# Kernel optimization log

Hardware: AMD Instinct MI355X
Metric: run time of the kernel (lower is better)

Reference implementation:

```python
import math
import jax, jax.numpy as jnp
from jax import lax
import numpy as np

jax.config.update("jax_enable_x64", True)  # original uses complex128 FFTs

MS_H = 5
MS_W = 5
EPS = 1e-8


def setup_inputs() -> dict:
    H = W = 512
    B = 32
    rng = np.random.default_rng(0)
    i = np.arange(H, dtype=np.float64)[:, None]
    j = np.arange(W, dtype=np.float64)[None, :]
    # smooth, strictly-positive template so NCC peak neighborhood is log-safe
    template = (2.0
                + np.exp(-(((i - H / 2) ** 2 + (j - W / 2) ** 2) / (2 * (H / 8.0) ** 2)))
                + 0.5 * np.cos(2 * np.pi * 3 * i / H) * np.cos(2 * np.pi * 5 * j / W)
                + 0.3 * np.sin(2 * np.pi * 7 * j / W + 1.0) * np.cos(2 * np.pi * 2 * i / H)
                ).astype(np.float32)
    frames = np.empty((B, H, W), np.float32)
    for b in range(B):
        dx, dy = rng.integers(-3, 4, size=2)
        frames[b] = np.roll(template, (int(dx), int(dy)), axis=(0, 1))
    frames += 0.02 * rng.standard_normal((B, H, W)).astype(np.float32)
    fr = jnp.asarray(frames)[None, :, :, :, None]  # [1, B, H, W, 1]
    return {"fr": fr, "template": jnp.asarray(template)}


def reference(fr, template):
    B = fr.shape[1]
    H, W = template.shape
    # ---- normalize_template ----
    template_zm = template - jnp.mean(template)
    template_var = jnp.sum(jnp.square(template_zm)) + EPS  # scalar
    # fft3d of [H,W,1] == 2D FFT over (H,W)
    target_freq = jnp.fft.fft2(template_zm.astype(jnp.complex128))  # [H,W]

    imgs = fr[0]  # [B,H,W,1]
    # ---- normalize_image ----
    k0, k1 = H - 2 * MS_W, W - 2 * MS_H
    imgs_zm = imgs - jnp.mean(imgs, axis=(1, 2), keepdims=True)
    x = imgs[:, :, :, 0]
    img_stack = jnp.stack([x, jnp.square(x)], axis=3)  # [B,H,W,2]
    localsum = lax.reduce_window(img_stack, jnp.array(0.0, img_stack.dtype), lax.add,
                                 (1, k0, k1, 1), (1, 1, 1, 1), 'VALID') / (k0 * k1)
    ls = localsum[:, :, :, 0:1]      # avg(x)   [B,11,11,1]
    ls_sq = localsum[:, :, :, 1:2]   # avg(x^2)
    imgs_var = ls_sq - jnp.square(ls) / (k0 * k1) + EPS
    imgs_var = jnp.where(imgs_var < 0, 0.0, imgs_var)

    denominator = jnp.sqrt(template_var * imgs_var)  # [B,11,11,1]

    # ---- FFT cross-correlation (fft3d over (batch,H,W) as in TF) ----
    fr_freq = jnp.fft.fftn(imgs_zm[:, :, :, 0].astype(jnp.complex128), axes=(0, 1, 2))
    img_product = fr_freq * jnp.conj(target_freq)[None]
    cc = jnp.abs(jnp.fft.ifftn(img_product, axes=(0, 1, 2))).astype(jnp.float32)
    rolled = jnp.roll(cc, (B, H // 2, W // 2), axis=(0, 1, 2))
    nominator = rolled[:, H // 2 - MS_W:H // 2 + MS_W + 1,
                       W // 2 - MS_H:W // 2 + MS_H + 1, None]  # [B,11,11,1]

    ncc = nominator / denominator
    ncc = jnp.where(jnp.isnan(ncc), 0.0, ncc)

    # ---- extract_fractional_peak ----
    Y = 2 * MS_H + 1
    nc = ncc[..., 0]  # [B,11,11]
    am = jnp.argmax(nc.reshape(B, -1), axis=1)
    sh_xi = am // Y
    sh_yi = am % Y
    sh_x_n = -(sh_xi - MS_H).astype(jnp.float32)
    sh_y_n = -(sh_yi - MS_W).astype(jnp.float32)
    l = jnp.log(nc)
    bb = jnp.arange(B)
    log_xm1_y = l[bb, sh_xi - 1, sh_yi]
    log_xp1_y = l[bb, sh_xi + 1, sh_yi]
    log_x_ym1 = l[bb, sh_xi, sh_yi - 1]
    log_x_yp1 = l[bb, sh_xi, sh_yi + 1]
    four_log_xy = 4.0 * l[bb, sh_xi, sh_yi]
    sh_x_n = sh_x_n - (log_xm1_y - log_xp1_y) / (2 * log_xm1_y - four_log_xy + 2 * log_xp1_y)
    sh_y_n = sh_y_n - (log_x_ym1 - log_x_yp1) / (2 * log_x_ym1 - four_log_xy + 2 * log_x_yp1)
    sh_x = sh_x_n  # [B]
    sh_y = sh_y_n

    # ---- apply_shifts_dft_tf(fr[0], [-sh_x, -sh_y]) ----
    # shifts tuple becomes (-sh_y, -sh_x, 0); sh_0 uses -shifts[0]=sh_y with Nr, sh_1 uses sh_x with Nc
    Nr = jnp.fft.ifftshift(jnp.arange(-math.floor(W / 2.0), math.ceil(W / 2.0))).astype(jnp.float32)  # [W]
    Nc = jnp.fft.ifftshift(jnp.arange(-math.floor(H / 2.0), math.ceil(H / 2.0))).astype(jnp.float32)  # [H]
    sh_tot = (sh_y[:, None, None] * Nr[None, None, :] / W
              + sh_x[:, None, None] * Nc[None, :, None] / H)  # [B,H,W]
    src_freq = jnp.fft.fftn(fr[0, :, :, :, 0].astype(jnp.complex128), axes=(1, 2))
    Greg = src_freq * jnp.exp(-1j * 2.0 * math.pi * sh_tot.astype(jnp.complex128))
    new_img = jnp.real(jnp.fft.ifftn(Greg, axes=(1, 2))).astype(jnp.float32)  # [B,H,W]

    out = jnp.transpose(new_img, (0, 2, 1)).reshape(B, H * W)
    return out
```

## Files before the change

### kernel.cpp

```cpp
#include <hip/hip_runtime.h>
#include <hip/hip_bf16.h>
#include <math.h>

#define NPIX 262144
#define PI_D 3.14159265358979323846264338327950288

typedef __attribute__((ext_vector_type(8))) short v8s;
typedef __attribute__((ext_vector_type(4))) float v4f;
typedef __attribute__((ext_vector_type(4))) unsigned short v4u;


__device__ inline unsigned short f2bf(float x){ return __bfloat16_as_ushort(__float2bfloat16(x)); }
__device__ inline float bf2f(unsigned short h){ return __bfloat162float(__ushort_as_bfloat16(h)); }

__global__ __launch_bounds__(256) void k_stats_part(const float* __restrict__ t, double* __restrict__ part){
    int base = blockIdx.x * 4096;
    double s = 0.0, s2 = 0.0;
    #pragma unroll
    for (int k = 0; k < 4; ++k){
        float4 v = *(const float4*)&t[base + k*1024 + threadIdx.x*4];
        s  += (double)v.x + (double)v.y + (double)v.z + (double)v.w;
        s2 += (double)v.x*v.x + (double)v.y*v.y + (double)v.z*v.z + (double)v.w*v.w;
    }
    __shared__ double rs[256], rs2[256];
    rs[threadIdx.x] = s; rs2[threadIdx.x] = s2; __syncthreads();
    for (int off = 128; off > 0; off >>= 1){
        if (threadIdx.x < off){ rs[threadIdx.x] += rs[threadIdx.x+off]; rs2[threadIdx.x] += rs2[threadIdx.x+off]; }
        __syncthreads();
    }
    if (threadIdx.x == 0){ part[blockIdx.x*2] = rs[0]; part[blockIdx.x*2+1] = rs2[0]; }
}

__global__ __launch_bounds__(64) void k_stats_final(const double* __restrict__ part, double* __restrict__ stats){
    double s = part[threadIdx.x*2], s2 = part[threadIdx.x*2+1];
    #pragma unroll
    for (int off = 32; off > 0; off >>= 1){
        s  += __shfl_down(s, off);
        s2 += __shfl_down(s2, off);
    }
    if (threadIdx.x == 0){
        stats[0] = s / (double)NPIX;
        stats[1] = s2 - s*s/(double)NPIX + 1e-8;
    }
}

__global__ __launch_bounds__(256) void k_tsplit(const float* __restrict__ tpl, const double* __restrict__ stats,
                                                unsigned short* __restrict__ tsp){
    float mean = (float)stats[0];
    int base = blockIdx.x * 1024 + threadIdx.x * 4;
    float4 v = *(const float4*)&tpl[base];
    v.x -= mean; v.y -= mean; v.z -= mean; v.w -= mean;
    unsigned short h0 = f2bf(v.x), h1 = f2bf(v.y), h2 = f2bf(v.z), h3 = f2bf(v.w);
    v4u hv = {h0, h1, h2, h3};
    v4u lv = {f2bf(v.x - bf2f(h0)), f2bf(v.y - bf2f(h1)), f2bf(v.z - bf2f(h2)), f2bf(v.w - bf2f(h3))};
    *(v4u*)&tsp[base] = hv;
    *(v4u*)&tsp[262144 + base] = lv;
}

__global__ __launch_bounds__(256) void k_winfin(const float* __restrict__ fr, const float* __restrict__ csum,
                                                const float* __restrict__ csum2, const double* __restrict__ stats,
                                                double* __restrict__ den){
    int b = blockIdx.x;
    const float* img = fr + (size_t)b * NPIX;
    __shared__ double fc[512], fc2[512];
    __shared__ double rsum[20], rsum2[20];
    __shared__ float E[20][20], E2[20][20];
    __shared__ double red[256], red2[256];
    int t = threadIdx.x;
    for (int c = t; c < 512; c += 256){
        double s = 0.0, s2 = 0.0;
        for (int k = 0; k < 64; ++k){
            size_t o = ((size_t)(b*64 + k) << 9) + c;
            s += (double)csum[o]; s2 += (double)csum2[o];
        }
        fc[c] = s; fc2[c] = s2;
    }
    if (t < 400){
        int i = t / 20, j = t % 20;
        int row = (i < 10) ? i : (i + 492);
        int col = (j < 10) ? j : (j + 492);
        float v = img[(row<<9) + col];
        E[i][j] = v; E2[i][j] = v*v;
    }
    __syncthreads();
    red[t] = fc[t] + fc[t+256];
    red2[t] = fc2[t] + fc2[t+256];
    __syncthreads();
    for (int off = 128; off > 0; off >>= 1){
        if (t < off){ red[t] += red[t+off]; red2[t] += red2[t+off]; }
        __syncthreads();
    }
    double F1 = red[0], F2 = red2[0];
    int lane = t & 63, wv = t >> 6;
    for (int e = wv; e < 20; e += 4){
        int row = (e < 10) ? e : (e + 492);
        double s = 0.0, s2 = 0.0;
        for (int c = lane; c < 512; c += 64){
            float v = img[(row<<9) + c];
            s += v; s2 += (double)v*v;
        }
        #pragma unroll
        for (int off = 32; off > 0; off >>= 1){ s += __shfl_down(s, off); s2 += __shfl_down(s2, off); }
        if (lane == 0){ rsum[e] = s; rsum2[e] = s2; }
    }
    __syncthreads();
    if (t < 121){
        int u = t / 11, v = t % 11;
        double S1 = F1, S2 = F2;
        for (int i = 0; i < u; ++i){ S1 -= rsum[i]; S2 -= rsum2[i]; }
        for (int k = 10+u; k < 20; ++k){ S1 -= rsum[k]; S2 -= rsum2[k]; }
        for (int j = 0; j < v; ++j){
            double cw = fc[j], cq = fc2[j];
            for (int i = 0; i < u; ++i){ cw -= E[i][j]; cq -= E2[i][j]; }
            for (int k = 10+u; k < 20; ++k){ cw -= E[k][j]; cq -= E2[k][j]; }
            S1 -= cw; S2 -= cq;
        }
        for (int jj = 10+v; jj < 20; ++jj){
            int col = jj + 492;
            double cw = fc[col], cq = fc2[col];
            for (int i = 0; i < u; ++i){ cw -= E[i][jj]; cq -= E2[i][jj]; }
            for (int k = 10+u; k < 20; ++k){ cw -= E[k][jj]; cq -= E2[k][jj]; }
            S1 -= cw; S2 -= cq;
        }
        const double K = 502.0*502.0;
        double ivar = S2/K - (S1*S1)/(K*K*K) + 1e-8;
        if (ivar < 0.0) ivar = 0.0;
        den[b*121 + u*11 + v] = sqrt(stats[1] * ivar);
    }
}

__global__ __launch_bounds__(256, 2) void k_ncc(const float* __restrict__ fr,
                                                const unsigned short* __restrict__ tsp,
                                                float* __restrict__ partial,
                                                float* __restrict__ csum, float* __restrict__ csum2,
                                                double* __restrict__ snn_part){
    int b = blockIdx.x >> 6, chunk = blockIdx.x & 63;
    int i0 = chunk << 3;
    int tid = threadIdx.x;
    __shared__ unsigned short Th[24][520], Tl[24][520];
    __shared__ unsigned short Xh[8][544], Xl[8][544];
    __shared__ float Dred[4][16][16];
    __shared__ double snred[4];
    for (int q = tid; q < 1536; q += 256){
        int r = q >> 6, c8 = (q & 63) << 3;
        int grow = (i0 - 5 + r + 512) & 511;
        *(float4*)&Th[r][c8] = *(const float4*)&tsp[((size_t)grow << 9) + c8];
        *(float4*)&Tl[r][c8] = *(const float4*)&tsp[262144 + ((size_t)grow << 9) + c8];
    }
    const float* img = fr + ((size_t)b << 18);
    for (int q = tid; q < 1088; q += 256){
        int r = q / 136, qq = q - r*136;
        int col = ((qq << 2) - 16) & 511;
        float4 v = *(const float4*)&img[((size_t)(i0 + r) << 9) + col];
        unsigned short h0 = f2bf(v.x), h1 = f2bf(v.y), h2 = f2bf(v.z), h3 = f2bf(v.w);
        v4u hv = {h0, h1, h2, h3};
        v4u lv = {f2bf(v.x - bf2f(h0)), f2bf(v.y - bf2f(h1)), f2bf(v.z - bf2f(h2)), f2bf(v.w - bf2f(h3))};
        *(v4u*)&Xh[r][qq << 2] = hv;
        *(v4u*)&Xl[r][qq << 2] = lv;
    }
    __syncthreads();
    int l = tid & 63, wv = tid >> 6;
    {
        int c0 = tid << 1;
        float s0=0.f, q0=0.f, s1=0.f, q1=0.f;
        double sn = 0.0;
        #pragma unroll
        for (int r = 0; r < 8; ++r){
            unsigned uh = *(const unsigned*)&Xh[r][c0 + 16];
            unsigned ul = *(const unsigned*)&Xl[r][c0 + 16];
            float v0 = bf2f((unsigned short)uh) + bf2f((unsigned short)ul);
            float v1 = bf2f((unsigned short)(uh >> 16)) + bf2f((unsigned short)(ul >> 16));
            s0 += v0; q0 += v0*v0; s1 += v1; q1 += v1*v1;
            float d = v0 - v1;
            sn += ((i0 + r) & 1) ? -(double)d : (double)d;
        }
        size_t o = ((size_t)(b*64 + chunk) << 9) + c0;
        float2 cs = {s0, s1}, cq = {q0, q1};
        *(float2*)&csum[o] = cs;
        *(float2*)&csum2[o] = cq;
        #pragma unroll
        for (int off = 32; off > 0; off >>= 1) sn += __shfl_down(sn, off);
        if (l == 0) snred[wv] = sn;
    }
    int lr = l & 15, lk = l >> 4;
    v4f acc = (v4f){0.f, 0.f, 0.f, 0.f};
    union UB { unsigned u[4]; v8s s; };
    int sbase = (lk << 3) - lr + 21;
    unsigned sh = (unsigned)((sbase & 1) << 4);
    #pragma unroll
    for (int ii = 0; ii < 2; ++ii){
        int ro = 2*wv + ii;
        const unsigned* xh32 = (const unsigned*)&Xh[ro][0];
        const unsigned* xl32 = (const unsigned*)&Xl[ro][0];
        #pragma unroll 1
        for (int ks = 0; ks < 16; ++ks){
            int ka = (ks << 5) + (lk << 3);
            v8s ah = *(v8s*)&Th[ro + lr][ka];
            v8s al = *(v8s*)&Tl[ro + lr][ka];
            int W = ((ks << 5) + sbase) >> 1;
            unsigned wh[5], wl[5];
            #pragma unroll
            for (int j = 0; j < 5; ++j){ wh[j] = xh32[W + j]; wl[j] = xl32[W + j]; }
            UB bh, bl;
            #pragma unroll
            for (int j = 0; j < 4; ++j){
                bh.u[j] = __builtin_amdgcn_alignbit(wh[j+1], wh[j], sh);
                bl.u[j] = __builtin_amdgcn_alignbit(wl[j+1], wl[j], sh);
            }
            acc = __builtin_amdgcn_mfma_f32_16x16x32_bf16(ah, bh.s, acc, 0, 0, 0);
            acc = __builtin_amdgcn_mfma_f32_16x16x32_bf16(al, bh.s, acc, 0, 0, 0);
            acc = __builtin_amdgcn_mfma_f32_16x16x32_bf16(ah, bl.s, acc, 0, 0, 0);
        }
    }
    #pragma unroll
    for (int r = 0; r < 4; ++r) Dred[wv][4*lk + r][lr] = acc[r];
    __syncthreads();
    if (tid < 121){
        int s0 = tid / 11, s1 = tid - s0*11;
        int dy = 10 - s0, dx = 10 - s1;
        partial[(size_t)(b*64 + chunk)*121 + tid] =
            Dred[0][dy][dx] + Dred[1][dy][dx] + Dred[2][dy][dx] + Dred[3][dy][dx];
    }
    if (tid == 0)
        snn_part[b*64 + chunk] = snred[0] + snred[1] + snred[2] + snred[3];
}

__global__ __launch_bounds__(128) void k_shifts(const float* __restrict__ partial, const double* __restrict__ den,
                                                const double* __restrict__ snn_part, double* __restrict__ shx,
                                                double* __restrict__ shy, float* __restrict__ c2){
    int b = blockIdx.x;
    __shared__ double l[121], nc[121];
    for (int e = threadIdx.x; e < 121; e += 128){
        double s = 0.0;
        for (int c = 0; c < 64; ++c) s += (double)partial[(size_t)(b*64 + c)*121 + e];
        double nom = fabs(s);
        double v = nom / den[b*121 + e];
        if (v != v) v = 0.0;
        nc[e] = v;
        l[e] = log(v);
    }
    __syncthreads();
    if (threadIdx.x == 0){
        int am = 0; double best = nc[0];
        for (int e = 1; e < 121; ++e) if (nc[e] > best){ best = nc[e]; am = e; }
        int u = am / 11, v = am % 11;
        double sx = -(double)(u - 5), sy = -(double)(v - 5);
        int um1 = u - 1; if (um1 < 0) um1 += 11; if (um1 > 10) um1 = 10;
        int up1 = u + 1; if (up1 > 10) up1 = 10;
        int vm1 = v - 1; if (vm1 < 0) vm1 += 11; if (vm1 > 10) vm1 = 10;
        int vp1 = v + 1; if (vp1 > 10) vp1 = 10;
        double l0x4 = 4.0 * l[u*11 + v];
        double lm = l[um1*11 + v], lp = l[up1*11 + v];
        sx -= (lm - lp) / (2.0*lm - l0x4 + 2.0*lp);
        double lm2 = l[u*11 + vm1], lp2 = l[u*11 + vp1];
        sy -= (lm2 - lp2) / (2.0*lm2 - l0x4 + 2.0*lp2);
        shx[b] = sx; shy[b] = sy;
        double snn = 0.0;
        for (int c = 0; c < 64; ++c) snn += snn_part[b*64 + c];
        double kx = sin(PI_D * sx) / 512.0, ky = sin(PI_D * sy) / 512.0;
        c2[b] = (float)(kx * ky * snn);
    }
}

__device__ inline double grekern(int t, double s){
    double u = (double)t - s;
    if (u > 256.0) u -= 512.0;
    double a = PI_D * u / 512.0;
    double sp = sin(a);
    double D;
    if (fabs(sp) < 1e-12) D = cos(PI_D * u) / cos(a);
    else D = sin(PI_D * u) / (512.0 * sp);
    return D * cos(a);
}

__global__ __launch_bounds__(256) void k_tables(const double* __restrict__ shx, const double* __restrict__ shy,
                                                unsigned short* __restrict__ gtab){
    int b = blockIdx.x;
    double sx = shx[b], sy = shy[b];
    unsigned short* g = gtab + ((size_t)b << 11);
    for (int t = threadIdx.x; t < 512; t += 256){
        float gy = (float)grekern(t, sy);
        float gx = (float)grekern(t, sx);
        unsigned short yh = f2bf(gy); unsigned short yl = f2bf(gy - bf2f(yh));
        unsigned short xh = f2bf(gx); unsigned short xl = f2bf(gx - bf2f(xh));
        g[t] = yh; g[512 + t] = yl; g[1024 + t] = xh; g[1536 + t] = xl;
    }
}

__global__ __launch_bounds__(256) void k_gemmA(const float* __restrict__ fr,
                                               const unsigned short* __restrict__ gtab,
                                               float* __restrict__ Cout, int b0, int swz){
    int bid = blockIdx.x;
    int lb, tile;
    if (swz){ int x = bid & 7; int r = bid >> 3; lb = (r >> 4)*8 + x; tile = r & 15; }
    else    { lb = bid >> 4; tile = bid & 15; }
    int mt = tile >> 2, nt = tile & 3;
    int tid = threadIdx.x;
    __shared__ unsigned short Ath[128][40], Atl[128][40];
    __shared__ unsigned short grh[1024], grl[1024];
    int bg = b0 + lb;
    const unsigned short* gax = gtab + ((size_t)bg << 11);
    for (int i = tid; i < 1024; i += 256){
        int src = (512 - (i & 511)) & 511;
        grh[i] = gax[src];
        grl[i] = gax[512 + src];
    }
    v4f acc[4][4];
    #pragma unroll
    for (int mi = 0; mi < 4; ++mi)
        #pragma unroll
        for (int ni = 0; ni < 4; ++ni) acc[mi][ni] = (v4f){0.f, 0.f, 0.f, 0.f};
    const float* img = fr + ((size_t)bg << 18) + (size_t)mt*128*512;
    int l = tid & 63, wv = tid >> 6;
    int wm = wv >> 1, wn = wv & 1;
    int lr = l & 15, lk = l >> 4;
    int colb = nt*128 + wn*64 + lr;
    unsigned sh = (unsigned)((colb & 1) << 4);
    const unsigned* grh32 = (const unsigned*)grh;
    const unsigned* grl32 = (const unsigned*)grl;
    union UB { unsigned u[4]; v8s s; };
    int rbase = tid >> 3, qoff = (tid & 7) << 2;
    float4 pf0 = *(const float4*)&img[(size_t)(rbase      )*512 + qoff];
    float4 pf1 = *(const float4*)&img[(size_t)(rbase + 32 )*512 + qoff];
    float4 pf2 = *(const float4*)&img[(size_t)(rbase + 64 )*512 + qoff];
    float4 pf3 = *(const float4*)&img[(size_t)(rbase + 96 )*512 + qoff];
    #pragma unroll 1
    for (int ks = 0; ks < 16; ++ks){
        __syncthreads();
        {
            float4 vv[4] = {pf0, pf1, pf2, pf3};
            #pragma unroll
            for (int p = 0; p < 4; ++p){
                float4 v = vv[p];
                unsigned short h0 = f2bf(v.x), h1 = f2bf(v.y), h2 = f2bf(v.z), h3 = f2bf(v.w);
                v4u hv = {h0, h1, h2, h3};
                v4u lv = {f2bf(v.x - bf2f(h0)), f2bf(v.y - bf2f(h1)), f2bf(v.z - bf2f(h2)), f2bf(v.w - bf2f(h3))};
                *(v4u*)&Ath[rbase + 32*p][qoff] = hv;
                *(v4u*)&Atl[rbase + 32*p][qoff] = lv;
            }
        }
        __syncthreads();
        v8s bhs[4], bls[4];
        #pragma unroll
        for (int ni = 0; ni < 4; ++ni){
            int f = ((ks << 5) + (lk << 3) - (colb + ni*16)) & 511;
            int W = f >> 1;
            unsigned wh[5], wl[5];
            #pragma unroll
            for (int j = 0; j < 5; ++j){ wh[j] = grh32[W + j]; wl[j] = grl32[W + j]; }
            UB bh, bl;
            #pragma unroll
            for (int j = 0; j < 4; ++j){
                bh.u[j] = __builtin_amdgcn_alignbit(wh[j+1], wh[j], sh);
                bl.u[j] = __builtin_amdgcn_alignbit(wl[j+1], wl[j], sh);
            }
            bhs[ni] = bh.s; bls[ni] = bl.s;
        }
        if (ks < 15){
            int c0 = ((ks + 1) << 5) + qoff;
            pf0 = *(const float4*)&img[(size_t)(rbase      )*512 + c0];
            pf1 = *(const float4*)&img[(size_t)(rbase + 32 )*512 + c0];
            pf2 = *(const float4*)&img[(size_t)(rbase + 64 )*512 + c0];
            pf3 = *(const float4*)&img[(size_t)(rbase + 96 )*512 + c0];
        }
        #pragma unroll
        for (int mi = 0; mi < 4; ++mi){
            int row = wm*64 + mi*16 + lr;
            v8s ah = *(v8s*)&Ath[row][lk*8];
            v8s al = *(v8s*)&Atl[row][lk*8];
            #pragma unroll
            for (int ni = 0; ni < 4; ++ni){
                acc[mi][ni] = __builtin_amdgcn_mfma_f32_16x16x32_bf16(ah, bhs[ni], acc[mi][ni], 0, 0, 0);
                acc[mi][ni] = __builtin_amdgcn_mfma_f32_16x16x32_bf16(al, bhs[ni], acc[mi][ni], 0, 0, 0);
                acc[mi][ni] = __builtin_amdgcn_mfma_f32_16x16x32_bf16(ah, bls[ni], acc[mi][ni], 0, 0, 0);
            }
        }
    }
    float* outp = Cout + ((size_t)bg << 18);
    int crow4 = lk * 4;
    #pragma unroll
    for (int mi = 0; mi < 4; ++mi)
        #pragma unroll
        for (int ni = 0; ni < 4; ++ni)
            #pragma unroll
            for (int rg = 0; rg < 4; ++rg){
                int row = mt*128 + wm*64 + mi*16 + crow4 + rg;
                int col = nt*128 + wn*64 + ni*16 + lr;
                outp[((size_t)row << 9) + col] = acc[mi][ni][rg];
            }
}

template<int CORR>
__global__ __launch_bounds__(256) void k_gemm(const unsigned short* __restrict__ Ahi,
                                              const unsigned short* __restrict__ Alo,
                                              const unsigned short* __restrict__ gtab, int axis,
                                              float* __restrict__ Cout,
                                              const float* __restrict__ c2, int b0, int swz){
    int bid = blockIdx.x;
    int lb, tile;
    if (swz){ int x = bid & 7; int r = bid >> 3; lb = (r >> 4)*8 + x; tile = r & 15; }
    else    { lb = bid >> 4; tile = bid & 15; }
    int mt = tile >> 2, nt = tile & 3;
    int tid = threadIdx.x;
    __shared__ unsigned short Ath[128][40], Atl[128][40];
    __shared__ unsigned short grh[1024], grl[1024];
    int bg = b0 + lb;
    const unsigned short* gax = gtab + ((size_t)bg << 11) + (axis << 10);
    for (int i = tid; i < 1024; i += 256){
        int src = (512 - (i & 511)) & 511;
        grh[i] = gax[src];
        grl[i] = gax[512 + src];
    }
    v4f acc[4][4];
    #pragma unroll
    for (int mi = 0; mi < 4; ++mi)
        #pragma unroll
        for (int ni = 0; ni < 4; ++ni) acc[mi][ni] = (v4f){0.f, 0.f, 0.f, 0.f};
    const unsigned short* Aph = Ahi + ((size_t)lb << 18) + (size_t)mt*128*512;
    const unsigned short* Apl = Alo + ((size_t)lb << 18) + (size_t)mt*128*512;
    int l = tid & 63, wv = tid >> 6;
    int wm = wv >> 1, wn = wv & 1;
    int lr = l & 15, lk = l >> 4;
    int colb = nt*128 + wn*64 + lr;
    unsigned sh = (unsigned)((colb & 1) << 4);
    int srow = tid >> 1, sc = (tid & 1) << 4;
    const unsigned* grh32 = (const unsigned*)grh;
    const unsigned* grl32 = (const unsigned*)grl;
    union UB { unsigned u[4]; v8s s; };
    size_t go0 = (size_t)srow*512 + sc;
    float4 ph0 = *(const float4*)&Aph[go0];
    float4 ph1 = *(const float4*)&Aph[go0 + 8];
    float4 pl0 = *(const float4*)&Apl[go0];
    float4 pl1 = *(const float4*)&Apl[go0 + 8];
    #pragma unroll 1
    for (int ks = 0; ks < 16; ++ks){
        __syncthreads();
        { *(float4*)&Ath[srow][sc]     = ph0;
          *(float4*)&Ath[srow][sc + 8] = ph1;
          *(float4*)&Atl[srow][sc]     = pl0;
          *(float4*)&Atl[srow][sc + 8] = pl1; }
        __syncthreads();
        v8s bhs[4], bls[4];
        #pragma unroll
        for (int ni = 0; ni < 4; ++ni){
            int f = ((ks << 5) + (lk << 3) - (colb + ni*16)) & 511;
            int W = f >> 1;
            unsigned wh[5], wl[5];
            #pragma unroll
            for (int j = 0; j < 5; ++j){ wh[j] = grh32[W + j]; wl[j] = grl32[W + j]; }
            UB bh, bl;
            #pragma unroll
            for (int j = 0; j < 4; ++j){
                bh.u[j] = __builtin_amdgcn_alignbit(wh[j+1], wh[j], sh);
                bl.u[j] = __builtin_amdgcn_alignbit(wl[j+1], wl[j], sh);
            }
            bhs[ni] = bh.s; bls[ni] = bl.s;
        }
        if (ks < 15){
            size_t go = (size_t)srow*512 + ((ks + 1) << 5) + sc;
            ph0 = *(const float4*)&Aph[go];
            ph1 = *(const float4*)&Aph[go + 8];
            pl0 = *(const float4*)&Apl[go];
            pl1 = *(const float4*)&Apl[go + 8];
        }
        #pragma unroll
        for (int mi = 0; mi < 4; ++mi){
            int row = wm*64 + mi*16 + lr;
            v8s ah = *(v8s*)&Ath[row][lk*8];
            v8s al = *(v8s*)&Atl[row][lk*8];
            #pragma unroll
            for (int ni = 0; ni < 4; ++ni){
                acc[mi][ni] = __builtin_amdgcn_mfma_f32_16x16x32_bf16(ah, bhs[ni], acc[mi][ni], 0, 0, 0);
                acc[mi][ni] = __builtin_amdgcn_mfma_f32_16x16x32_bf16(al, bhs[ni], acc[mi][ni], 0, 0, 0);
                acc[mi][ni] = __builtin_amdgcn_mfma_f32_16x16x32_bf16(ah, bls[ni], acc[mi][ni], 0, 0, 0);
            }
        }
    }
    float cc = CORR ? c2[bg] : 0.f;
    float* outp = Cout + ((size_t)bg << 18);
    int crow4 = lk * 4;
    #pragma unroll
    for (int mi = 0; mi < 4; ++mi)
        #pragma unroll
        for (int ni = 0; ni < 4; ++ni)
            #pragma unroll
            for (int rg = 0; rg < 4; ++rg){
                int row = mt*128 + wm*64 + mi*16 + crow4 + rg;
                int col = nt*128 + wn*64 + ni*16 + lr;
                float v = acc[mi][ni][rg];
                if (CORR) v -= ((row + col) & 1) ? -cc : cc;
                outp[((size_t)row << 9) + col] = v;
            }
}

__global__ __launch_bounds__(256) void k_transpose2(const float* __restrict__ Y,
                                                    unsigned short* __restrict__ Thi,
                                                    unsigned short* __restrict__ Tlo, int b0){
    int lb = blockIdx.x >> 8, tb = blockIdx.x & 255;
    int tx = (tb & 15) << 5, ty = ((tb >> 4) & 15) << 5;
    const float* src = Y + (((size_t)(b0 + lb)) << 18);
    unsigned short* dh = Thi + (((size_t)lb) << 18);
    unsigned short* dl = Tlo + (((size_t)lb) << 18);
    __shared__ float tile[32][33];
    int col = threadIdx.x & 31, rw = threadIdx.x >> 5;
    #pragma unroll
    for (int k = 0; k < 4; ++k){
        int ry = rw + k*8;
        tile[ry][col] = src[((size_t)(ty + ry) << 9) + tx + col];
    }
    __syncthreads();
    #pragma unroll
    for (int k = 0; k < 4; ++k){
        int ry = rw + k*8;
        float v = tile[col][ry];
        unsigned short h = f2bf(v);
        size_t o = ((size_t)(tx + ry) << 9) + ty + col;
        dh[o] = h;
        dl[o] = f2bf(v - bf2f(h));
    }
}

extern "C" void kernel_launch(void* const* d_in, const int* in_sizes, int n_in,
                              void* d_out, int out_size, void* d_ws, size_t ws_size,
                              hipStream_t stream){
    (void)in_sizes; (void)n_in; (void)out_size;
    const float* fr  = (const float*)d_in[0];
    const float* tpl = (const float*)d_in[1];
    float* out = (float*)d_out;
    char* ws = (char*)d_ws;

    double* stats  = (double*)(ws + 0);
    double* spart  = (double*)(ws + 64);
    double* den    = (double*)(ws + 2048);
    double* snnp   = (double*)(ws + 33280);
    double* shx    = (double*)(ws + 49664);
    double* shy    = (double*)(ws + 49920);
    float*  c2     = (float*) (ws + 50176);
    float*  part   = (float*) (ws + 50304);
    unsigned short* gtab = (unsigned short*)(ws + 1041536);
    unsigned short* tsp  = (unsigned short*)(ws + 1172608);
    float*  csum   = (float*) (ws + 2221184);
    float*  csum2  = (float*) (ws + 6415488);

    const size_t CB = 10609792;
    long long avail = ((long long)ws_size - (long long)CB) / (1ll << 20);
    int NC = (int)avail; if (NC > 32) NC = 32; if (NC < 1) NC = 1;
    if (NC >= 8) NC &= ~7;
    int swz = (NC % 8 == 0) ? 1 : 0;

    unsigned short* YThi = (unsigned short*)(ws + CB);
    unsigned short* YTlo = YThi + (size_t)NC*262144;

    k_stats_part<<<64, 256, 0, stream>>>(tpl, spart);
    k_stats_final<<<1, 64, 0, stream>>>(spart, stats);
    k_tsplit<<<256, 256, 0, stream>>>(tpl, stats, tsp);
    k_ncc<<<2048, 256, 0, stream>>>(fr, tsp, part, csum, csum2, snnp);
    k_winfin<<<32, 256, 0, stream>>>(fr, csum, csum2, stats, den);
    k_shifts<<<32, 128, 0, stream>>>(part, den, snnp, shx, shy, c2);
    k_tables<<<32, 256, 0, stream>>>(shx, shy, gtab);

    for (int b0 = 0; b0 < 32; b0 += NC){
        int nb = (32 - b0 < NC) ? (32 - b0) : NC;
        int sw = (swz && (nb % 8 == 0)) ? 1 : 0;
        k_gemmA<<<nb*16, 256, 0, stream>>>(fr, gtab, out, b0, sw);
        k_transpose2<<<nb*256, 256, 0, stream>>>(out, YThi, YTlo, b0);
        k_gemm<1><<<nb*16, 256, 0, stream>>>(YThi, YTlo, gtab, 1, out, c2, b0, sw);
    }
}
```

Before: 169.1 us.

## Fuse transpose and bf16 hi/lo split into first GEMM epilogue

The first GEMM now transposes its accumulator tile through shared memory and writes the bf16 hi/lo split planes directly, so the separate transpose kernel goes away. This removes a full fp32 write and read of the intermediate per batch, plus one launch per chunk. In exchange the epilogue gets four sync-separated staging passes and extra shared memory, which may lower occupancy.

```diff
diff --git a/kernel.cpp b/kernel.cpp
--- a/kernel.cpp
+++ b/kernel.cpp
@@ -289,7 +289,8 @@
 
 __global__ __launch_bounds__(256) void k_gemmA(const float* __restrict__ fr,
                                                const unsigned short* __restrict__ gtab,
-                                               float* __restrict__ Cout, int b0, int swz){
+                                               unsigned short* __restrict__ YThi,
+                                               unsigned short* __restrict__ YTlo, int b0, int swz){
     int bid = blockIdx.x;
     int lb, tile;
     if (swz){ int x = bid & 7; int r = bid >> 3; lb = (r >> 4)*8 + x; tile = r & 15; }
@@ -298,6 +299,7 @@
     int tid = threadIdx.x;
     __shared__ unsigned short Ath[128][40], Atl[128][40];
     __shared__ unsigned short grh[1024], grl[1024];
+    __shared__ unsigned P[32][136];
     int bg = b0 + lb;
     const unsigned short* gax = gtab + ((size_t)bg << 11);
     for (int i = tid; i < 1024; i += 256){
@@ -376,18 +378,50 @@
             }
         }
     }
-    float* outp = Cout + ((size_t)bg << 18);
+    unsigned short* dsth = YThi + ((size_t)lb << 18);
+    unsigned short* dstl = YTlo + ((size_t)lb << 18);
     int crow4 = lk * 4;
-    #pragma unroll
-    for (int mi = 0; mi < 4; ++mi)
-        #pragma unroll
-        for (int ni = 0; ni < 4; ++ni)
-            #pragma unroll
-            for (int rg = 0; rg < 4; ++rg){
-                int row = mt*128 + wm*64 + mi*16 + crow4 + rg;
-                int col = nt*128 + wn*64 + ni*16 + lr;
-                outp[((size_t)row << 9) + col] = acc[mi][ni][rg];
-            }
+    #pragma unroll 1
+    for (int s = 0; s < 4; ++s){
+        __syncthreads();
+        if (wn == (s >> 1)){
+            #pragma unroll
+            for (int ni2 = 0; ni2 < 2; ++ni2){
+                int ni = ((s & 1) << 1) + ni2;
+                int c_l = (ni2 << 4) + lr;
+                #pragma unroll
+                for (int mi = 0; mi < 4; ++mi)
+                    #pragma unroll
+                    for (int rg = 0; rg < 4; ++rg){
+                        int r_l = wm*64 + mi*16 + crow4 + rg;
+                        float v = acc[mi][ni][rg];
+                        unsigned short h = f2bf(v);
+                        unsigned short lo = f2bf(v - bf2f(h));
+                        P[c_l][r_l] = (unsigned)h | ((unsigned)lo << 16);
+                    }
+            }
+        }
+        __syncthreads();
+        {
+            int c_l = tid >> 3, seg = (tid & 7) << 4;
+            unsigned w[16];
+            #pragma unroll
+            for (int q = 0; q < 4; ++q)
+                *(uint4*)&w[4*q] = *(const uint4*)&P[c_l][seg + 4*q];
+            unsigned short hv[16], lv[16];
+            #pragma unroll
+            for (int j = 0; j < 16; ++j){ hv[j] = (unsigned short)w[j]; lv[j] = (unsigned short)(w[j] >> 16); }
+            size_t o = ((size_t)(nt*128 + s*32 + c_l) << 9) + mt*128 + seg;
+            *(v4u*)&dsth[o]     = *(v4u*)&hv[0];
+            *(v4u*)&dsth[o + 4] = *(v4u*)&hv[4];
+            *(v4u*)&dsth[o + 8] = *(v4u*)&hv[8];
+            *(v4u*)&dsth[o +12] = *(v4u*)&hv[12];
+            *(v4u*)&dstl[o]     = *(v4u*)&lv[0];
+            *(v4u*)&dstl[o + 4] = *(v4u*)&lv[4];
+            *(v4u*)&dstl[o + 8] = *(v4u*)&lv[8];
+            *(v4u*)&dstl[o +12] = *(v4u*)&lv[12];
+        }
+    }
 }
 
 template<int CORR>
@@ -493,33 +527,6 @@
             }
 }
 
-__global__ __launch_bounds__(256) void k_transpose2(const float* __restrict__ Y,
-                                                    unsigned short* __restrict__ Thi,
-                                                    unsigned short* __restrict__ Tlo, int b0){
-    int lb = blockIdx.x >> 8, tb = blockIdx.x & 255;
-    int tx = (tb & 15) << 5, ty = ((tb >> 4) & 15) << 5;
-    const float* src = Y + (((size_t)(b0 + lb)) << 18);
-    unsigned short* dh = Thi + (((size_t)lb) << 18);
-    unsigned short* dl = Tlo + (((size_t)lb) << 18);
-    __shared__ float tile[32][33];
-    int col = threadIdx.x & 31, rw = threadIdx.x >> 5;
-    #pragma unroll
-    for (int k = 0; k < 4; ++k){
-        int ry = rw + k*8;
-        tile[ry][col] = src[((size_t)(ty + ry) << 9) + tx + col];
-    }
-    __syncthreads();
-    #pragma unroll
-    for (int k = 0; k < 4; ++k){
-        int ry = rw + k*8;
-        float v = tile[col][ry];
-        unsigned short h = f2bf(v);
-        size_t o = ((size_t)(tx + ry) << 9) + ty + col;
-        dh[o] = h;
-        dl[o] = f2bf(v - bf2f(h));
-    }
-}
-
 extern "C" void kernel_launch(void* const* d_in, const int* in_sizes, int n_in,
                               void* d_out, int out_size, void* d_ws, size_t ws_size,
                               hipStream_t stream){
@@ -562,8 +569,7 @@
     for (int b0 = 0; b0 < 32; b0 += NC){
         int nb = (32 - b0 < NC) ? (32 - b0) : NC;
         int sw = (swz && (nb % 8 == 0)) ? 1 : 0;
-        k_gemmA<<<nb*16, 256, 0, stream>>>(fr, gtab, out, b0, sw);
-        k_transpose2<<<nb*256, 256, 0, stream>>>(out, YThi, YTlo, b0);
+        k_gemmA<<<nb*16, 256, 0, stream>>>(fr, gtab, YThi, YTlo, b0, sw);
         k_gemm<1><<<nb*16, 256, 0, stream>>>(YThi, YTlo, gtab, 1, out, c2, b0, sw);
     }
 }
```

Measured after the change: 221.1 us. 1.31x slower.
